# Performance work log

Measured on AMD Instinct MI355X. Metric: run time of the kernel, lower is better.

Reference implementation:

```python
import jax, jax.numpy as jnp
import numpy as np

N_ATOMS = 4096
CUTOFF = 5.0
BOX = 30.0  # cubic box edge length (Angstrom)


def setup_inputs() -> dict:
    key = jax.random.key(0)
    positions = jax.random.uniform(key, (N_ATOMS, 3), dtype=jnp.float32) * BOX
    cell = jnp.eye(3, dtype=jnp.float32) * BOX
    pbc = jnp.zeros((3,), dtype=bool)  # no PBC -> shifts branch is empty
    return {"positions": positions, "cell": cell, "pbc": pbc}


def reference(positions, cell, pbc):
    # pbc is all-False, so shifts = empty (center-cell pairs only), matching
    # the `torch.all(pbc == 0)` branch of the original module. cell is then
    # unused in the math.
    N = positions.shape[0]
    # combinations(arange(N)) -> all i<j pairs (static shapes)
    ii, jj = jnp.triu_indices(N, k=1)                      # [P], P = N(N-1)/2
    Rij = positions[ii] - positions[jj]                    # [P, 3]
    dist = jnp.linalg.norm(Rij, axis=1)                    # [P]
    in_cutoff = dist < CUTOFF                              # [P] bool

    # bidirectional pairs: (i->j with -Rij) then (j->i with +Rij), as in
    # bi_idx_i = cat(idx_i, idx_j), bi_Rij = cat(-Rij, Rij)
    bi_i = jnp.concatenate([ii, jj])                       # [2P]
    bi_j = jnp.concatenate([jj, ii])                       # [2P]
    bi_Rij = jnp.concatenate([-Rij, Rij], axis=0)          # [2P, 3]
    bi_mask = jnp.concatenate([in_cutoff, in_cutoff])      # [2P]

    # JAX needs static shapes: instead of nonzero-compaction, push invalid
    # (out-of-cutoff) pairs to the end with sentinel key N, then stable-sort
    # by idx_i exactly like torch.argsort(bi_idx_i) on the filtered set.
    sort_key = jnp.where(bi_mask, bi_i, N)                 # [2P]
    order = jnp.argsort(sort_key, stable=True)             # [2P]

    mask_s = bi_mask[order]                                # [2P]
    idx_i = jnp.where(mask_s, bi_i[order], N)              # sentinel N in padding
    idx_j = jnp.where(mask_s, bi_j[order], N)
    Rij_s = bi_Rij[order] * mask_s[:, None]                # zero padding rows
    cell_offset = jnp.zeros((bi_i.shape[0], 3), dtype=jnp.int32)  # no PBC
    num_pairs = jnp.sum(mask_s.astype(jnp.int32))          # valid-pair count
    return idx_i, idx_j, Rij_s, cell_offset, mask_s, num_pairs
```

## Files before the change

kernel.cpp:

```cpp
#include <hip/hip_runtime.h>


#define NA 4096
static constexpr long long PP = (long long)NA * (NA - 1) / 2;
static constexpr long long TP = 2 * PP;

__device__ __forceinline__ float dist2_exact(float dx, float dy, float dz) {
    return __fadd_rn(__fadd_rn(__fmul_rn(dx, dx), __fmul_rn(dy, dy)),
                     __fmul_rn(dz, dz));
}

__global__ void fill_kernel(float4* __restrict__ out4, long long n4, long long idx4) {
    long long stride = (long long)gridDim.x * blockDim.x;
    for (long long i = (long long)blockIdx.x * blockDim.x + threadIdx.x; i < n4; i += stride) {
        float v = (i < idx4) ? 4096.0f : 0.0f;
        out4[i] = make_float4(v, v, v, v);
    }
}

__global__ void count_kernel(const float* __restrict__ pos, int* __restrict__ cnt) {
    int wave = (int)(((long long)blockIdx.x * blockDim.x + threadIdx.x) >> 6);
    int lane = threadIdx.x & 63;
    if (wave >= NA) return;
    float ax = pos[3 * wave + 0], ay = pos[3 * wave + 1], az = pos[3 * wave + 2];
    int c = 0;
    for (int base = 0; base < NA; base += 64) {
        int p = base + lane;
        float dx = pos[3 * p + 0] - ax;
        float dy = pos[3 * p + 1] - ay;
        float dz = pos[3 * p + 2] - az;
        float d2 = dist2_exact(dx, dy, dz);
        if (p != wave && __fsqrt_rn(d2) < 5.0f) c++;
    }
    for (int off = 32; off; off >>= 1) c += __shfl_down(c, off, 64);
    if (lane == 0) cnt[wave] = c;
}

__global__ void scan_kernel(const int* __restrict__ cnt, int* __restrict__ off,
                            float* __restrict__ out_np) {
    __shared__ int sdata[1024];
    int tid = threadIdx.x;
    int v[4];
    int s = 0;
    for (int k = 0; k < 4; k++) { v[k] = cnt[tid * 4 + k]; s += v[k]; }
    sdata[tid] = s;
    __syncthreads();
    for (int d = 1; d < 1024; d <<= 1) {
        int t = (tid >= d) ? sdata[tid - d] : 0;
        __syncthreads();
        sdata[tid] += t;
        __syncthreads();
    }
    int excl = (tid == 0) ? 0 : sdata[tid - 1];
    for (int k = 0; k < 4; k++) { off[tid * 4 + k] = excl; excl += v[k]; }
    if (tid == 1023) out_np[0] = (float)sdata[1023];
}

__global__ void scatter_kernel(const float* __restrict__ pos, const int* __restrict__ off,
                               float* __restrict__ out) {
    int wave = (int)(((long long)blockIdx.x * blockDim.x + threadIdx.x) >> 6);
    int lane = threadIdx.x & 63;
    if (wave >= NA) return;
    int a = wave;
    float ax = pos[3 * a + 0], ay = pos[3 * a + 1], az = pos[3 * a + 2];
    int o = off[a];
    for (int phase = 0; phase < 2; ++phase) {
        int lo = (phase == 0) ? a + 1 : 0;
        int hi = (phase == 0) ? NA : a;
        for (int base = lo & ~63; base < hi; base += 64) {
            int p = base + lane;
            bool valid = (p >= lo) && (p < hi);
            float px = 0.f, py = 0.f, pz = 0.f;
            if (valid) {
                px = pos[3 * p + 0]; py = pos[3 * p + 1]; pz = pos[3 * p + 2];
                float d2 = dist2_exact(px - ax, py - ay, pz - az);
                valid = __fsqrt_rn(d2) < 5.0f;
            }
            unsigned long long m = __ballot(valid);
            if (valid) {
                int idx = o + __popcll(m & ((1ull << lane) - 1ull));
                out[idx] = (float)a;
                out[TP + idx] = (float)p;
                long long r = 2 * TP + 3LL * idx;
                out[r + 0] = px - ax;
                out[r + 1] = py - ay;
                out[r + 2] = pz - az;
                out[8 * TP + idx] = 1.0f;
            }
            o += __popcll(m);
        }
    }
}

extern "C" void kernel_launch(void* const* d_in, const int* in_sizes, int n_in,
                              void* d_out, int out_size, void* d_ws, size_t ws_size,
                              hipStream_t stream) {
    const float* pos = (const float*)d_in[0];
    float* out = (float*)d_out;
    int* cnt = (int*)d_ws;
    int* off = cnt + NA;

    const long long n4 = (18 * PP) / 4;
    const long long idx4 = PP;

    count_kernel<<<NA / 4, 256, 0, stream>>>(pos, cnt);
    scan_kernel<<<1, 1024, 0, stream>>>(cnt, off, out + 18 * PP);
    fill_kernel<<<2048, 256, 0, stream>>>((float4*)out, n4, idx4);
    scatter_kernel<<<NA / 4, 256, 0, stream>>>(pos, off, out);
}
```

Before: 184.1 us.

## Fuse fill with count kernel and replace scan with per-wave prefix sums

Merges the output fill and the per-atom neighbor count into one launch, using block index ranges so the memory-bound fill runs beside the compute-bound count. Removes the single-block scan kernel: each scatter wave sums the counts of all lower atoms itself to get its offset. Fill loops use 32-bit indices and split the sentinel and zero regions into two loops. This cuts two launches and a serial scan, at the cost of redundant O(N^2) count reads spread across scatter waves.

```diff
diff --git a/kernel.cpp b/kernel.cpp
--- a/kernel.cpp
+++ b/kernel.cpp
@@ -4,66 +4,57 @@
 #define NA 4096
 static constexpr long long PP = (long long)NA * (NA - 1) / 2;
 static constexpr long long TP = 2 * PP;
+static constexpr int FILL_BLOCKS = 2048;
+static constexpr int COUNT_BLOCKS = NA / 4;
 
 __device__ __forceinline__ float dist2_exact(float dx, float dy, float dz) {
     return __fadd_rn(__fadd_rn(__fmul_rn(dx, dx), __fmul_rn(dy, dy)),
                      __fmul_rn(dz, dz));
 }
 
-__global__ void fill_kernel(float4* __restrict__ out4, long long n4, long long idx4) {
-    long long stride = (long long)gridDim.x * blockDim.x;
-    for (long long i = (long long)blockIdx.x * blockDim.x + threadIdx.x; i < n4; i += stride) {
-        float v = (i < idx4) ? 4096.0f : 0.0f;
-        out4[i] = make_float4(v, v, v, v);
+__global__ void fill_count_kernel(const float* __restrict__ pos, int* __restrict__ cnt,
+                                  float4* __restrict__ out4) {
+    int bid = blockIdx.x;
+    if (bid < FILL_BLOCKS) {
+        const int n4 = (int)(18 * PP / 4);
+        const int idx4 = (int)PP;
+        const int stride = FILL_BLOCKS * 256;
+        const int i0 = bid * 256 + threadIdx.x;
+        const float4 sent = make_float4(4096.f, 4096.f, 4096.f, 4096.f);
+        const float4 zero = make_float4(0.f, 0.f, 0.f, 0.f);
+        for (int i = i0; i < idx4; i += stride) out4[i] = sent;
+        for (int i = idx4 + i0; i < n4; i += stride) out4[i] = zero;
+    } else {
+        int cb = bid - FILL_BLOCKS;
+        int wid = threadIdx.x >> 6, lane = threadIdx.x & 63;
+        int a = cb * 4 + wid;
+        float ax = pos[3 * a + 0], ay = pos[3 * a + 1], az = pos[3 * a + 2];
+        int c = 0;
+        for (int base = 0; base < NA; base += 64) {
+            int p = base + lane;
+            float dx = pos[3 * p + 0] - ax;
+            float dy = pos[3 * p + 1] - ay;
+            float dz = pos[3 * p + 2] - az;
+            if (p != a && __fsqrt_rn(dist2_exact(dx, dy, dz)) < 5.0f) c++;
+        }
+        for (int off = 32; off; off >>= 1) c += __shfl_down(c, off, 64);
+        if (lane == 0) cnt[a] = c;
     }
 }
 
-__global__ void count_kernel(const float* __restrict__ pos, int* __restrict__ cnt) {
-    int wave = (int)(((long long)blockIdx.x * blockDim.x + threadIdx.x) >> 6);
-    int lane = threadIdx.x & 63;
-    if (wave >= NA) return;
-    float ax = pos[3 * wave + 0], ay = pos[3 * wave + 1], az = pos[3 * wave + 2];
-    int c = 0;
-    for (int base = 0; base < NA; base += 64) {
-        int p = base + lane;
-        float dx = pos[3 * p + 0] - ax;
-        float dy = pos[3 * p + 1] - ay;
-        float dz = pos[3 * p + 2] - az;
-        float d2 = dist2_exact(dx, dy, dz);
-        if (p != wave && __fsqrt_rn(d2) < 5.0f) c++;
-    }
-    for (int off = 32; off; off >>= 1) c += __shfl_down(c, off, 64);
-    if (lane == 0) cnt[wave] = c;
-}
+__global__ void scatter_kernel(const float* __restrict__ pos, const int* __restrict__ cnt,
+                               float* __restrict__ out) {
+    int wid = threadIdx.x >> 6, lane = threadIdx.x & 63;
+    int a = blockIdx.x * 4 + wid;
+    float ax = pos[3 * a + 0], ay = pos[3 * a + 1], az = pos[3 * a + 2];
 
-__global__ void scan_kernel(const int* __restrict__ cnt, int* __restrict__ off,
-                            float* __restrict__ out_np) {
-    __shared__ int sdata[1024];
-    int tid = threadIdx.x;
-    int v[4];
     int s = 0;
-    for (int k = 0; k < 4; k++) { v[k] = cnt[tid * 4 + k]; s += v[k]; }
-    sdata[tid] = s;
-    __syncthreads();
-    for (int d = 1; d < 1024; d <<= 1) {
-        int t = (tid >= d) ? sdata[tid - d] : 0;
-        __syncthreads();
-        sdata[tid] += t;
-        __syncthreads();
-    }
-    int excl = (tid == 0) ? 0 : sdata[tid - 1];
-    for (int k = 0; k < 4; k++) { off[tid * 4 + k] = excl; excl += v[k]; }
-    if (tid == 1023) out_np[0] = (float)sdata[1023];
-}
+    for (int i = lane; i < a; i += 64) s += cnt[i];
+    for (int off = 32; off; off >>= 1) s += __shfl_down(s, off, 64);
+    int o = __shfl(s, 0, 64);
 
-__global__ void scatter_kernel(const float* __restrict__ pos, const int* __restrict__ off,
-                               float* __restrict__ out) {
-    int wave = (int)(((long long)blockIdx.x * blockDim.x + threadIdx.x) >> 6);
-    int lane = threadIdx.x & 63;
-    if (wave >= NA) return;
-    int a = wave;
-    float ax = pos[3 * a + 0], ay = pos[3 * a + 1], az = pos[3 * a + 2];
-    int o = off[a];
+    if (a == NA - 1 && lane == 0) out[18 * PP] = (float)(o + cnt[a]);
+
     for (int phase = 0; phase < 2; ++phase) {
         int lo = (phase == 0) ? a + 1 : 0;
         int hi = (phase == 0) ? NA : a;
@@ -73,8 +64,7 @@
             float px = 0.f, py = 0.f, pz = 0.f;
             if (valid) {
                 px = pos[3 * p + 0]; py = pos[3 * p + 1]; pz = pos[3 * p + 2];
-                float d2 = dist2_exact(px - ax, py - ay, pz - az);
-                valid = __fsqrt_rn(d2) < 5.0f;
+                valid = __fsqrt_rn(dist2_exact(px - ax, py - ay, pz - az)) < 5.0f;
             }
             unsigned long long m = __ballot(valid);
             if (valid) {
@@ -98,13 +88,7 @@
     const float* pos = (const float*)d_in[0];
     float* out = (float*)d_out;
     int* cnt = (int*)d_ws;
-    int* off = cnt + NA;
 
-    const long long n4 = (18 * PP) / 4;
-    const long long idx4 = PP;
-
-    count_kernel<<<NA / 4, 256, 0, stream>>>(pos, cnt);
-    scan_kernel<<<1, 1024, 0, stream>>>(cnt, off, out + 18 * PP);
-    fill_kernel<<<2048, 256, 0, stream>>>((float4*)out, n4, idx4);
-    scatter_kernel<<<NA / 4, 256, 0, stream>>>(pos, off, out);
+    fill_count_kernel<<<FILL_BLOCKS + COUNT_BLOCKS, 256, 0, stream>>>(pos, cnt, (float4*)out);
+    scatter_kernel<<<COUNT_BLOCKS, 256, 0, stream>>>(pos, cnt, out);
 }
```

Measured after the change: 182.0 us. No clear change (-1.1%).
